# Kernel optimization log

Hardware: AMD Instinct MI355X
Metric: run time of the kernel (lower is better)

The kernel has to match this reference:

```python
import jax, jax.numpy as jnp
import numpy as np

EPS = 1e-3  # BatchNorm eps from module init
N, C_IN, K = 200000, 256, 27
C_MID = C_IN // 4  # bottleneck expansion = 4


def batch_norm(h, gamma, beta):
    # BatchNorm1d in training mode: biased batch stats over the node dim
    mean = jnp.mean(h, axis=0)
    var = jnp.var(h, axis=0)
    return (h - mean) * jax.lax.rsqrt(var + EPS) * gamma + beta


def setup_inputs() -> dict:
    key = jax.random.key(0)
    ks = jax.random.split(key, 8)
    x = jax.random.normal(ks[0], (N, C_IN), dtype=jnp.float32)
    neigh = jax.random.randint(ks[1], (N, K), 0, N)  # 27-neighbor octree table
    # conv weights (no bias; BN follows). Fan-in scaled init.
    W1 = jax.random.normal(ks[2], (C_IN, C_MID), dtype=jnp.float32) / np.sqrt(C_IN)
    W2 = jax.random.normal(ks[3], (K, C_MID, C_MID), dtype=jnp.float32) / np.sqrt(K * C_MID)
    W3 = jax.random.normal(ks[4], (C_MID, C_IN), dtype=jnp.float32) / np.sqrt(C_MID)
    g1 = jnp.ones((C_MID,), jnp.float32); b1 = jnp.zeros((C_MID,), jnp.float32)
    g2 = jnp.ones((C_MID,), jnp.float32); b2 = jnp.zeros((C_MID,), jnp.float32)
    g3 = jnp.ones((C_IN,), jnp.float32); b3 = jnp.zeros((C_IN,), jnp.float32)
    return {"x": x, "neigh": neigh, "depth": 6,
            "W1": W1, "g1": g1, "b1": b1,
            "W2": W2, "g2": g2, "b2": b2,
            "W3": W3, "g3": g3, "b3": b3}


def reference(x, neigh, depth, W1, g1, b1, W2, g2, b2, W3, g3, b3):
    identity = x
    # conv_bn_relu1: 1x1 octree conv -> BN -> ReLU
    h = jax.nn.relu(batch_norm(x @ W1, g1, b1))  # [N, C_MID]
    # conv_bn_relu2: 3x3 octree conv (27-neighbor gather) -> BN -> ReLU
    gathered = h[neigh]                          # [N, 27, C_MID] irregular gather
    h = jnp.einsum('nkc,kcd->nd', gathered, W2)  # [N, C_MID]
    h = jax.nn.relu(batch_norm(h, g2, b2))
    # conv3: 1x1 octree conv back to C_IN, then BN + residual + ReLU
    h = batch_norm(h @ W3, g3, b3)               # [N, C_IN]
    return jax.nn.relu(h + identity)
```

## Files before the change

### kernel.cpp

```cpp
#include <hip/hip_runtime.h>
#include <stdint.h>

#define N_NODES 200000
#define C_INN   256
#define C_MIDD  64
#define KNB     27

typedef unsigned short u16;
typedef __attribute__((ext_vector_type(8))) short short8;
typedef __attribute__((ext_vector_type(4))) float floatx4;

__device__ inline float bf2f(u16 u) {
  union { uint32_t i; float f; } v; v.i = ((uint32_t)u) << 16; return v.f;
}
__device__ inline u16 f2bf(float f) {
  union { float f; uint32_t i; } v; v.f = f;
  uint32_t lsb = (v.i >> 16) & 1u;
  uint32_t r = v.i + 0x7fffu + lsb;
  return (u16)(r >> 16);
}

__global__ void prep_kernel(const float* __restrict__ W1, const float* __restrict__ W2,
                            const float* __restrict__ W3,
                            u16* __restrict__ w1t, u16* __restrict__ w2t,
                            u16* __restrict__ w3t, float* __restrict__ stats) {
  int tid = blockIdx.x * blockDim.x + threadIdx.x;
  int nth = gridDim.x * blockDim.x;
  for (int i = tid; i < 1536; i += nth) stats[i] = 0.f;
  for (int i = tid; i < 256 * 64; i += nth) {
    int d = i >> 8, k = i & 255;
    w1t[i] = f2bf(W1[k * 64 + d]);
  }
  for (int i = tid; i < 27 * 64 * 64; i += nth) {
    int kn = i >> 12, r = i & 4095, d = r >> 6, c = r & 63;
    w2t[i] = f2bf(W2[kn * 4096 + c * 64 + d]);
  }
  for (int i = tid; i < 256 * 64; i += nth) {
    int d = i >> 6, k = i & 63;
    w3t[i] = f2bf(W3[k * 256 + d]);
  }
}

#define PAD1 136
__global__ __launch_bounds__(256) void gemm1_kernel(const float* __restrict__ x,
                                                    const u16* __restrict__ w1t,
                                                    u16* __restrict__ y1) {
  __shared__ u16 Als[64 * PAD1];
  __shared__ u16 Bls[64 * PAD1];
  int t = threadIdx.x;
  long long rowBase = (long long)blockIdx.x * 64;
  int w = t >> 6, lane = t & 63;
  int m = lane & 15, q = lane >> 4;
  floatx4 acc[4] = {};

  for (int kh = 0; kh < 2; kh++) {
    if (kh) __syncthreads();
    #pragma unroll
    for (int j = 0; j < 8; j++) {
      int lin = j * 256 + t;
      int r = lin >> 5, c4 = lin & 31;
      floatx4 v = ((const floatx4*)x)[(rowBase + r) * 64 + kh * 32 + c4];
      ushort4 u;
      u.x = f2bf(v[0]); u.y = f2bf(v[1]); u.z = f2bf(v[2]); u.w = f2bf(v[3]);
      *(ushort4*)&Als[r * PAD1 + c4 * 4] = u;
    }
    #pragma unroll
    for (int j = 0; j < 4; j++) {
      int lin = j * 256 + t;
      int n = lin >> 4, c8 = lin & 15;
      uint4 u = ((const uint4*)w1t)[n * 32 + kh * 16 + c8];
      *(uint4*)&Bls[n * PAD1 + c8 * 8] = u;
    }
    __syncthreads();
    #pragma unroll
    for (int kc = 0; kc < 4; kc++) {
      short8 af = *(const short8*)&Als[(w * 16 + m) * PAD1 + kc * 32 + q * 8];
      #pragma unroll
      for (int tt = 0; tt < 4; tt++) {
        short8 bf = *(const short8*)&Bls[(tt * 16 + m) * PAD1 + kc * 32 + q * 8];
        acc[tt] = __builtin_amdgcn_mfma_f32_16x16x32_bf16(af, bf, acc[tt], 0, 0, 0);
      }
    }
  }
  long long base = rowBase + w * 16;
  #pragma unroll
  for (int tt = 0; tt < 4; tt++)
    #pragma unroll
    for (int r = 0; r < 4; r++)
      y1[(base + q * 4 + r) * 64 + tt * 16 + m] = f2bf(acc[tt][r]);
}

#define PAD2 72
__global__ __launch_bounds__(256) void gemm2_kernel(const u16* __restrict__ h1,
                                                    const int* __restrict__ neigh,
                                                    const u16* __restrict__ w2t,
                                                    u16* __restrict__ y2) {
  __shared__ u16 Als[64 * PAD2];
  __shared__ u16 Bls[64 * PAD2];
  __shared__ int nidx[64 * 27];
  int t = threadIdx.x;
  long long rowBase = (long long)blockIdx.x * 64;
  #pragma unroll
  for (int j = 0; j < 7; j++) {
    int lin = j * 256 + t;
    if (lin < 64 * 27) nidx[lin] = neigh[rowBase * 27 + lin];
  }
  int w = t >> 6, lane = t & 63;
  int m = lane & 15, q = lane >> 4;
  floatx4 acc[4] = {};

  for (int k = 0; k < KNB; k++) {
    __syncthreads();
    #pragma unroll
    for (int j = 0; j < 2; j++) {
      int lin = j * 256 + t;
      int r = lin >> 3, c8 = lin & 7;
      long long src = (long long)nidx[r * 27 + k] * 8 + c8;
      *(uint4*)&Als[r * PAD2 + c8 * 8] = ((const uint4*)h1)[src];
      *(uint4*)&Bls[r * PAD2 + c8 * 8] = ((const uint4*)w2t)[k * 512 + lin];
    }
    __syncthreads();
    #pragma unroll
    for (int kc = 0; kc < 2; kc++) {
      short8 af = *(const short8*)&Als[(w * 16 + m) * PAD2 + kc * 32 + q * 8];
      #pragma unroll
      for (int tt = 0; tt < 4; tt++) {
        short8 bf = *(const short8*)&Bls[(tt * 16 + m) * PAD2 + kc * 32 + q * 8];
        acc[tt] = __builtin_amdgcn_mfma_f32_16x16x32_bf16(af, bf, acc[tt], 0, 0, 0);
      }
    }
  }
  long long base = rowBase + w * 16;
  #pragma unroll
  for (int tt = 0; tt < 4; tt++)
    #pragma unroll
    for (int r = 0; r < 4; r++)
      y2[(base + q * 4 + r) * 64 + tt * 16 + m] = f2bf(acc[tt][r]);
}

#define PAD3 72
__global__ __launch_bounds__(256) void gemm3_kernel(const u16* __restrict__ h2,
                                                    const u16* __restrict__ w3t,
                                                    float* __restrict__ y3) {
  __shared__ u16 Als[64 * PAD3];
  __shared__ u16 Bls[256 * PAD3];
  int t = threadIdx.x;
  long long rowBase = (long long)blockIdx.x * 64;
  #pragma unroll
  for (int j = 0; j < 2; j++) {
    int lin = j * 256 + t;
    int r = lin >> 3, c8 = lin & 7;
    *(uint4*)&Als[r * PAD3 + c8 * 8] = ((const uint4*)h2)[rowBase * 8 + lin];
  }
  #pragma unroll
  for (int j = 0; j < 8; j++) {
    int lin = j * 256 + t;
    int n = lin >> 3, c8 = lin & 7;
    *(uint4*)&Bls[n * PAD3 + c8 * 8] = ((const uint4*)w3t)[lin];
  }
  __syncthreads();
  int w = t >> 6, lane = t & 63;
  int m = lane & 15, q = lane >> 4;
  floatx4 acc[16] = {};
  short8 af0 = *(const short8*)&Als[(w * 16 + m) * PAD3 + q * 8];
  short8 af1 = *(const short8*)&Als[(w * 16 + m) * PAD3 + 32 + q * 8];
  #pragma unroll
  for (int tt = 0; tt < 16; tt++) {
    short8 b0 = *(const short8*)&Bls[(tt * 16 + m) * PAD3 + q * 8];
    short8 b1 = *(const short8*)&Bls[(tt * 16 + m) * PAD3 + 32 + q * 8];
    acc[tt] = __builtin_amdgcn_mfma_f32_16x16x32_bf16(af0, b0, acc[tt], 0, 0, 0);
    acc[tt] = __builtin_amdgcn_mfma_f32_16x16x32_bf16(af1, b1, acc[tt], 0, 0, 0);
  }
  long long base = rowBase + w * 16;
  #pragma unroll
  for (int tt = 0; tt < 16; tt++)
    #pragma unroll
    for (int r = 0; r < 4; r++)
      y3[(base + q * 4 + r) * 256 + tt * 16 + m] = acc[tt][r];
}

template <int C, bool BF>
__global__ __launch_bounds__(256) void stats_kernel(const void* __restrict__ yv,
                                                    float* __restrict__ sums) {
  const int RPB = 256 / C;
  int t = threadIdx.x;
  int c = t % C, rg = t / C;
  float s = 0.f, sq = 0.f;
  for (long long row = (long long)blockIdx.x * RPB + rg; row < N_NODES;
       row += (long long)gridDim.x * RPB) {
    float v = BF ? bf2f(((const u16*)yv)[row * C + c])
                 : ((const float*)yv)[row * C + c];
    s += v; sq += v * v;
  }
  __shared__ float ls[256], lq[256];
  ls[t] = s; lq[t] = sq;
  __syncthreads();
  if (t < C) {
    float S = 0.f, Q = 0.f;
    for (int g = 0; g < RPB; g++) { S += ls[g * C + t]; Q += lq[g * C + t]; }
    atomicAdd(&sums[t], S);
    atomicAdd(&sums[C + t], Q);
  }
}

__global__ void finalize_kernel(const float* __restrict__ sums, const float* __restrict__ g,
                                const float* __restrict__ b, float* __restrict__ ac, int C) {
  int t = threadIdx.x;
  if (t < C) {
    float inv = 1.f / (float)N_NODES;
    float mean = sums[t] * inv;
    float var = sums[C + t] * inv - mean * mean;
    float a = g[t] * rsqrtf(var + 1e-3f);
    ac[t] = a;
    ac[C + t] = b[t] - mean * a;
  }
}

__global__ __launch_bounds__(256) void apply_bn_relu_kernel(u16* __restrict__ y,
                                                            const float* __restrict__ ac) {
  __shared__ float a[64], cc[64];
  int t = threadIdx.x;
  if (t < 64) { a[t] = ac[t]; cc[t] = ac[64 + t]; }
  __syncthreads();
  const long long total = (long long)N_NODES * 64 / 8;
  for (long long i = (long long)blockIdx.x * 256 + t; i < total;
       i += (long long)gridDim.x * 256) {
    uint4 u = ((uint4*)y)[i];
    int c0 = (int)((i & 7) * 8);
    u16* us = (u16*)&u;
    #pragma unroll
    for (int j = 0; j < 8; j++) {
      float v = bf2f(us[j]);
      v = fmaf(a[c0 + j], v, cc[c0 + j]);
      us[j] = f2bf(fmaxf(v, 0.f));
    }
    ((uint4*)y)[i] = u;
  }
}

__global__ __launch_bounds__(256) void epilogue_kernel(float* __restrict__ y3,
                                                       const float* __restrict__ x,
                                                       const float* __restrict__ ac) {
  __shared__ float a[256], cc[256];
  int t = threadIdx.x;
  a[t] = ac[t]; cc[t] = ac[256 + t];
  __syncthreads();
  const long long total = (long long)N_NODES * 256 / 4;
  for (long long i = (long long)blockIdx.x * 256 + t; i < total;
       i += (long long)gridDim.x * 256) {
    floatx4 v = ((floatx4*)y3)[i];
    floatx4 xi = ((const floatx4*)x)[i];
    int c0 = (int)((i & 63) * 4);
    #pragma unroll
    for (int j = 0; j < 4; j++) {
      float r = fmaf(a[c0 + j], v[j], cc[c0 + j]) + xi[j];
      v[j] = fmaxf(r, 0.f);
    }
    ((floatx4*)y3)[i] = v;
  }
}

extern "C" void kernel_launch(void* const* d_in, const int* in_sizes, int n_in,
                              void* d_out, int out_size, void* d_ws, size_t ws_size,
                              hipStream_t stream) {
  (void)in_sizes; (void)n_in; (void)out_size; (void)ws_size;
  const float* x  = (const float*)d_in[0];
  const int* neigh = (const int*)d_in[1];
  const float* W1 = (const float*)d_in[3];
  const float* g1 = (const float*)d_in[4];
  const float* b1 = (const float*)d_in[5];
  const float* W2 = (const float*)d_in[6];
  const float* g2 = (const float*)d_in[7];
  const float* b2 = (const float*)d_in[8];
  const float* W3 = (const float*)d_in[9];
  const float* g3 = (const float*)d_in[10];
  const float* b3 = (const float*)d_in[11];

  char* ws = (char*)d_ws;
  u16* h1  = (u16*)(ws);
  u16* h2  = (u16*)(ws + 25600000LL);
  u16* w1t = (u16*)(ws + 51200000LL);
  u16* w2t = (u16*)(ws + 51232768LL);
  u16* w3t = (u16*)(ws + 51453952LL);
  float* stats = (float*)(ws + 51486720LL);
  float* s1 = stats,        *ac1 = stats + 128;
  float* s2 = stats + 256,  *ac2 = stats + 384;
  float* s3 = stats + 512,  *ac3 = stats + 1024;
  float* y3 = (float*)d_out;

  const int MB = N_NODES / 64;

  prep_kernel<<<256, 256, 0, stream>>>(W1, W2, W3, w1t, w2t, w3t, stats);

  gemm1_kernel<<<MB, 256, 0, stream>>>(x, w1t, h1);
  stats_kernel<64, true><<<1024, 256, 0, stream>>>(h1, s1);
  finalize_kernel<<<1, 256, 0, stream>>>(s1, g1, b1, ac1, 64);
  apply_bn_relu_kernel<<<2048, 256, 0, stream>>>(h1, ac1);

  gemm2_kernel<<<MB, 256, 0, stream>>>(h1, neigh, w2t, h2);
  stats_kernel<64, true><<<1024, 256, 0, stream>>>(h2, s2);
  finalize_kernel<<<1, 256, 0, stream>>>(s2, g2, b2, ac2, 64);
  apply_bn_relu_kernel<<<2048, 256, 0, stream>>>(h2, ac2);

  gemm3_kernel<<<MB, 256, 0, stream>>>(h2, w3t, y3);
  stats_kernel<256, false><<<2048, 256, 0, stream>>>(y3, s3);
  finalize_kernel<<<1, 256, 0, stream>>>(s3, g3, b3, ac3, 256);
  epilogue_kernel<<<4096, 256, 0, stream>>>(y3, x, ac3);
}
```

Baseline: 764.2 us.

## Fuse BN stats into GEMMs and derive BN3 stats from Gram matrix

```diff
diff --git a/kernel.cpp b/kernel.cpp
--- a/kernel.cpp
+++ b/kernel.cpp
@@ -5,6 +5,8 @@
 #define C_INN   256
 #define C_MIDD  64
 #define KNB     27
+#define MB_TILES 3125
+#define GRAM_BLOCKS 512
 
 typedef unsigned short u16;
 typedef __attribute__((ext_vector_type(8))) short short8;
@@ -26,7 +28,7 @@
                             u16* __restrict__ w3t, float* __restrict__ stats) {
   int tid = blockIdx.x * blockDim.x + threadIdx.x;
   int nth = gridDim.x * blockDim.x;
-  for (int i = tid; i < 1536; i += nth) stats[i] = 0.f;
+  for (int i = tid; i < 512; i += nth) stats[i] = 0.f;
   for (int i = tid; i < 256 * 64; i += nth) {
     int d = i >> 8, k = i & 255;
     w1t[i] = f2bf(W1[k * 64 + d]);
@@ -44,7 +46,8 @@
 #define PAD1 136
 __global__ __launch_bounds__(256) void gemm1_kernel(const float* __restrict__ x,
                                                     const u16* __restrict__ w1t,
-                                                    u16* __restrict__ y1) {
+                                                    u16* __restrict__ y1,
+                                                    float* __restrict__ s) {
   __shared__ u16 Als[64 * PAD1];
   __shared__ u16 Bls[64 * PAD1];
   int t = threadIdx.x;
@@ -88,13 +91,43 @@
     #pragma unroll
     for (int r = 0; r < 4; r++)
       y1[(base + q * 4 + r) * 64 + tt * 16 + m] = f2bf(acc[tt][r]);
+
+  float sv[4], qv[4];
+  #pragma unroll
+  for (int tt = 0; tt < 4; tt++) {
+    float sl = 0.f, ql = 0.f;
+    #pragma unroll
+    for (int r = 0; r < 4; r++) { float v = acc[tt][r]; sl += v; ql += v * v; }
+    sl += __shfl_xor(sl, 16); sl += __shfl_xor(sl, 32);
+    ql += __shfl_xor(ql, 16); ql += __shfl_xor(ql, 32);
+    sv[tt] = sl; qv[tt] = ql;
+  }
+  __syncthreads();
+  float* sred = (float*)Als;
+  float* qred = sred + 256;
+  if (q == 0) {
+    #pragma unroll
+    for (int tt = 0; tt < 4; tt++) {
+      sred[w * 64 + tt * 16 + m] = sv[tt];
+      qred[w * 64 + tt * 16 + m] = qv[tt];
+    }
+  }
+  __syncthreads();
+  if (t < 64) {
+    float S = 0.f, Q = 0.f;
+    #pragma unroll
+    for (int g = 0; g < 4; g++) { S += sred[g * 64 + t]; Q += qred[g * 64 + t]; }
+    atomicAdd(&s[t], S);
+    atomicAdd(&s[64 + t], Q);
+  }
 }
 
 #define PAD2 72
 __global__ __launch_bounds__(256) void gemm2_kernel(const u16* __restrict__ h1,
                                                     const int* __restrict__ neigh,
                                                     const u16* __restrict__ w2t,
-                                                    u16* __restrict__ y2) {
+                                                    u16* __restrict__ y2,
+                                                    float* __restrict__ s) {
   __shared__ u16 Als[64 * PAD2];
   __shared__ u16 Bls[64 * PAD2];
   __shared__ int nidx[64 * 27];
@@ -136,70 +169,34 @@
     #pragma unroll
     for (int r = 0; r < 4; r++)
       y2[(base + q * 4 + r) * 64 + tt * 16 + m] = f2bf(acc[tt][r]);
-}
-
-#define PAD3 72
-__global__ __launch_bounds__(256) void gemm3_kernel(const u16* __restrict__ h2,
-                                                    const u16* __restrict__ w3t,
-                                                    float* __restrict__ y3) {
-  __shared__ u16 Als[64 * PAD3];
-  __shared__ u16 Bls[256 * PAD3];
-  int t = threadIdx.x;
-  long long rowBase = (long long)blockIdx.x * 64;
-  #pragma unroll
-  for (int j = 0; j < 2; j++) {
-    int lin = j * 256 + t;
-    int r = lin >> 3, c8 = lin & 7;
-    *(uint4*)&Als[r * PAD3 + c8 * 8] = ((const uint4*)h2)[rowBase * 8 + lin];
-  }
-  #pragma unroll
-  for (int j = 0; j < 8; j++) {
-    int lin = j * 256 + t;
-    int n = lin >> 3, c8 = lin & 7;
-    *(uint4*)&Bls[n * PAD3 + c8 * 8] = ((const uint4*)w3t)[lin];
-  }
-  __syncthreads();
-  int w = t >> 6, lane = t & 63;
-  int m = lane & 15, q = lane >> 4;
-  floatx4 acc[16] = {};
-  short8 af0 = *(const short8*)&Als[(w * 16 + m) * PAD3 + q * 8];
-  short8 af1 = *(const short8*)&Als[(w * 16 + m) * PAD3 + 32 + q * 8];
-  #pragma unroll
-  for (int tt = 0; tt < 16; tt++) {
-    short8 b0 = *(const short8*)&Bls[(tt * 16 + m) * PAD3 + q * 8];
-    short8 b1 = *(const short8*)&Bls[(tt * 16 + m) * PAD3 + 32 + q * 8];
-    acc[tt] = __builtin_amdgcn_mfma_f32_16x16x32_bf16(af0, b0, acc[tt], 0, 0, 0);
-    acc[tt] = __builtin_amdgcn_mfma_f32_16x16x32_bf16(af1, b1, acc[tt], 0, 0, 0);
-  }
-  long long base = rowBase + w * 16;
-  #pragma unroll
-  for (int tt = 0; tt < 16; tt++)
-    #pragma unroll
-    for (int r = 0; r < 4; r++)
-      y3[(base + q * 4 + r) * 256 + tt * 16 + m] = acc[tt][r];
-}
-
-template <int C, bool BF>
-__global__ __launch_bounds__(256) void stats_kernel(const void* __restrict__ yv,
-                                                    float* __restrict__ sums) {
-  const int RPB = 256 / C;
-  int t = threadIdx.x;
-  int c = t % C, rg = t / C;
-  float s = 0.f, sq = 0.f;
-  for (long long row = (long long)blockIdx.x * RPB + rg; row < N_NODES;
-       row += (long long)gridDim.x * RPB) {
-    float v = BF ? bf2f(((const u16*)yv)[row * C + c])
-                 : ((const float*)yv)[row * C + c];
-    s += v; sq += v * v;
-  }
-  __shared__ float ls[256], lq[256];
-  ls[t] = s; lq[t] = sq;
-  __syncthreads();
-  if (t < C) {
+
+  float sv[4], qv[4];
+  #pragma unroll
+  for (int tt = 0; tt < 4; tt++) {
+    float sl = 0.f, ql = 0.f;
+    #pragma unroll
+    for (int r = 0; r < 4; r++) { float v = acc[tt][r]; sl += v; ql += v * v; }
+    sl += __shfl_xor(sl, 16); sl += __shfl_xor(sl, 32);
+    ql += __shfl_xor(ql, 16); ql += __shfl_xor(ql, 32);
+    sv[tt] = sl; qv[tt] = ql;
+  }
+  __syncthreads();
+  float* sred = (float*)Als;
+  float* qred = sred + 256;
+  if (q == 0) {
+    #pragma unroll
+    for (int tt = 0; tt < 4; tt++) {
+      sred[w * 64 + tt * 16 + m] = sv[tt];
+      qred[w * 64 + tt * 16 + m] = qv[tt];
+    }
+  }
+  __syncthreads();
+  if (t < 64) {
     float S = 0.f, Q = 0.f;
-    for (int g = 0; g < RPB; g++) { S += ls[g * C + t]; Q += lq[g * C + t]; }
-    atomicAdd(&sums[t], S);
-    atomicAdd(&sums[C + t], Q);
+    #pragma unroll
+    for (int g = 0; g < 4; g++) { S += sred[g * 64 + t]; Q += qred[g * 64 + t]; }
+    atomicAdd(&s[t], S);
+    atomicAdd(&s[64 + t], Q);
   }
 }
 
@@ -238,25 +235,154 @@
   }
 }
 
-__global__ __launch_bounds__(256) void epilogue_kernel(float* __restrict__ y3,
-                                                       const float* __restrict__ x,
-                                                       const float* __restrict__ ac) {
-  __shared__ float a[256], cc[256];
-  int t = threadIdx.x;
-  a[t] = ac[t]; cc[t] = ac[256 + t];
-  __syncthreads();
-  const long long total = (long long)N_NODES * 256 / 4;
-  for (long long i = (long long)blockIdx.x * 256 + t; i < total;
-       i += (long long)gridDim.x * 256) {
-    floatx4 v = ((floatx4*)y3)[i];
-    floatx4 xi = ((const floatx4*)x)[i];
-    int c0 = (int)((i & 63) * 4);
-    #pragma unroll
-    for (int j = 0; j < 4; j++) {
-      float r = fmaf(a[c0 + j], v[j], cc[c0 + j]) + xi[j];
-      v[j] = fmaxf(r, 0.f);
-    }
-    ((floatx4*)y3)[i] = v;
+#define PADG 72
+__global__ __launch_bounds__(256) void gram_kernel(const u16* __restrict__ h2,
+                                                   float* __restrict__ Gpart,
+                                                   float* __restrict__ cspart) {
+  __shared__ u16 T[64 * PADG];
+  int t = threadIdx.x;
+  int w = t >> 6, lane = t & 63;
+  int m = lane & 15, q = lane >> 4;
+  const int c8 = t & 7;
+  floatx4 acc[4] = {};
+  float csl[8] = {};
+  for (int tile = blockIdx.x; tile < MB_TILES; tile += gridDim.x) {
+    __syncthreads();
+    #pragma unroll
+    for (int j = 0; j < 2; j++) {
+      int lin = j * 256 + t;
+      int r = lin >> 3;
+      uint4 u = ((const uint4*)h2)[(long long)tile * 512 + lin];
+      u16* us = (u16*)&u;
+      #pragma unroll
+      for (int e = 0; e < 8; e++) {
+        csl[e] += bf2f(us[e]);
+        T[(c8 * 8 + e) * PADG + r] = us[e];
+      }
+    }
+    __syncthreads();
+    #pragma unroll
+    for (int kc = 0; kc < 2; kc++) {
+      short8 af = *(const short8*)&T[(w * 16 + m) * PADG + kc * 32 + q * 8];
+      #pragma unroll
+      for (int tt = 0; tt < 4; tt++) {
+        short8 bf = *(const short8*)&T[(tt * 16 + m) * PADG + kc * 32 + q * 8];
+        acc[tt] = __builtin_amdgcn_mfma_f32_16x16x32_bf16(af, bf, acc[tt], 0, 0, 0);
+      }
+    }
+  }
+  long long b = blockIdx.x;
+  #pragma unroll
+  for (int tt = 0; tt < 4; tt++)
+    #pragma unroll
+    for (int r = 0; r < 4; r++)
+      Gpart[b * 4096 + (w * 16 + q * 4 + r) * 64 + tt * 16 + m] = acc[tt][r];
+  __syncthreads();
+  float* cred = (float*)T;
+  #pragma unroll
+  for (int e = 0; e < 8; e++) cred[t * 8 + e] = csl[e];
+  __syncthreads();
+  if (t < 64) {
+    float S = 0.f;
+    for (int g = 0; g < 32; g++) S += cred[((g << 3) | (t >> 3)) * 8 + (t & 7)];
+    cspart[b * 64 + t] = S;
+  }
+}
+
+__global__ void greduce_kernel(const float* __restrict__ Gpart,
+                               const float* __restrict__ cspart,
+                               float* __restrict__ G, float* __restrict__ cs) {
+  int idx = blockIdx.x * 64 + threadIdx.x;
+  if (idx < 4096) {
+    float S = 0.f;
+    for (int b = 0; b < GRAM_BLOCKS; b++) S += Gpart[b * 4096 + idx];
+    G[idx] = S;
+  } else if (idx < 4160) {
+    int c = idx - 4096;
+    float S = 0.f;
+    for (int b = 0; b < GRAM_BLOCKS; b++) S += cspart[b * 64 + c];
+    cs[c] = S;
+  }
+}
+
+__global__ void finalize3_kernel(const float* __restrict__ G, const float* __restrict__ cs,
+                                 const u16* __restrict__ w3t, const float* __restrict__ g3,
+                                 const float* __restrict__ b3, float* __restrict__ ac3) {
+  __shared__ float Gs[4096];
+  __shared__ float css[64];
+  int t = threadIdx.x;
+  for (int i = t; i < 4096; i += 256) Gs[i] = G[i];
+  if (t < 64) css[t] = cs[t];
+  __syncthreads();
+  float wv[64];
+  #pragma unroll
+  for (int k = 0; k < 64; k++) wv[k] = bf2f(w3t[t * 64 + k]);
+  const float invN = 1.f / (float)N_NODES;
+  float mean = 0.f;
+  #pragma unroll
+  for (int k = 0; k < 64; k++) mean += css[k] * wv[k];
+  mean *= invN;
+  float qf = 0.f;
+  #pragma unroll
+  for (int k = 0; k < 64; k++) {
+    float tmp = 0.f;
+    #pragma unroll
+    for (int k2 = 0; k2 < 64; k2++) tmp += Gs[k * 64 + k2] * wv[k2];
+    qf += wv[k] * tmp;
+  }
+  float var = qf * invN - mean * mean;
+  float a = g3[t] * rsqrtf(var + 1e-3f);
+  ac3[t] = a;
+  ac3[256 + t] = b3[t] - mean * a;
+}
+
+#define PAD3 72
+__global__ __launch_bounds__(256) void gemm3e_kernel(const u16* __restrict__ h2,
+                                                     const u16* __restrict__ w3t,
+                                                     const float* __restrict__ ac,
+                                                     const float* __restrict__ x,
+                                                     float* __restrict__ out) {
+  __shared__ u16 Als[64 * PAD3];
+  __shared__ u16 Bls[256 * PAD3];
+  __shared__ float aS[256], cS[256];
+  int t = threadIdx.x;
+  aS[t] = ac[t]; cS[t] = ac[256 + t];
+  long long rowBase = (long long)blockIdx.x * 64;
+  #pragma unroll
+  for (int j = 0; j < 2; j++) {
+    int lin = j * 256 + t;
+    int r = lin >> 3, c8 = lin & 7;
+    *(uint4*)&Als[r * PAD3 + c8 * 8] = ((const uint4*)h2)[rowBase * 8 + lin];
+  }
+  #pragma unroll
+  for (int j = 0; j < 8; j++) {
+    int lin = j * 256 + t;
+    int n = lin >> 3, c8 = lin & 7;
+    *(uint4*)&Bls[n * PAD3 + c8 * 8] = ((const uint4*)w3t)[lin];
+  }
+  __syncthreads();
+  int w = t >> 6, lane = t & 63;
+  int m = lane & 15, q = lane >> 4;
+  floatx4 acc[16] = {};
+  short8 af0 = *(const short8*)&Als[(w * 16 + m) * PAD3 + q * 8];
+  short8 af1 = *(const short8*)&Als[(w * 16 + m) * PAD3 + 32 + q * 8];
+  #pragma unroll
+  for (int tt = 0; tt < 16; tt++) {
+    short8 b0 = *(const short8*)&Bls[(tt * 16 + m) * PAD3 + q * 8];
+    short8 b1 = *(const short8*)&Bls[(tt * 16 + m) * PAD3 + 32 + q * 8];
+    acc[tt] = __builtin_amdgcn_mfma_f32_16x16x32_bf16(af0, b0, acc[tt], 0, 0, 0);
+    acc[tt] = __builtin_amdgcn_mfma_f32_16x16x32_bf16(af1, b1, acc[tt], 0, 0, 0);
+  }
+  long long base = rowBase + w * 16;
+  #pragma unroll
+  for (int r = 0; r < 4; r++) {
+    long long row = base + q * 4 + r;
+    #pragma unroll
+    for (int tt = 0; tt < 16; tt++) {
+      int col = tt * 16 + m;
+      float v = fmaf(aS[col], acc[tt][r], cS[col]) + x[row * 256 + col];
+      out[row * 256 + col] = fmaxf(v, 0.f);
+    }
   }
 }
 
@@ -283,27 +409,27 @@
   u16* w2t = (u16*)(ws + 51232768LL);
   u16* w3t = (u16*)(ws + 51453952LL);
   float* stats = (float*)(ws + 51486720LL);
-  float* s1 = stats,        *ac1 = stats + 128;
-  float* s2 = stats + 256,  *ac2 = stats + 384;
-  float* s3 = stats + 512,  *ac3 = stats + 1024;
-  float* y3 = (float*)d_out;
-
-  const int MB = N_NODES / 64;
+  float* s1  = stats,       *ac1 = stats + 128;
+  float* s2  = stats + 256, *ac2 = stats + 384;
+  float* G   = stats + 512;
+  float* cs3 = stats + 4608;
+  float* ac3 = stats + 4672;
+  float* Gpart  = (float*)(ws + 51507456LL);
+  float* cspart = (float*)(ws + 59896064LL);
+  float* out = (float*)d_out;
 
   prep_kernel<<<256, 256, 0, stream>>>(W1, W2, W3, w1t, w2t, w3t, stats);
 
-  gemm1_kernel<<<MB, 256, 0, stream>>>(x, w1t, h1);
-  stats_kernel<64, true><<<1024, 256, 0, stream>>>(h1, s1);
+  gemm1_kernel<<<MB_TILES, 256, 0, stream>>>(x, w1t, h1, s1);
   finalize_kernel<<<1, 256, 0, stream>>>(s1, g1, b1, ac1, 64);
   apply_bn_relu_kernel<<<2048, 256, 0, stream>>>(h1, ac1);
 
-  gemm2_kernel<<<MB, 256, 0, stream>>>(h1, neigh, w2t, h2);
-  stats_kernel<64, true><<<1024, 256, 0, stream>>>(h2, s2);
+  gemm2_kernel<<<MB_TILES, 256, 0, stream>>>(h1, neigh, w2t, h2, s2);
   finalize_kernel<<<1, 256, 0, stream>>>(s2, g2, b2, ac2, 64);
   apply_bn_relu_kernel<<<2048, 256, 0, stream>>>(h2, ac2);
 
-  gemm3_kernel<<<MB, 256, 0, stream>>>(h2, w3t, y3);
-  stats_kernel<256, false><<<2048, 256, 0, stream>>>(y3, s3);
-  finalize_kernel<<<1, 256, 0, stream>>>(s3, g3, b3, ac3, 256);
-  epilogue_kernel<<<4096, 256, 0, stream>>>(y3, x, ac3);
-}
+  gram_kernel<<<GRAM_BLOCKS, 256, 0, stream>>>(h2, Gpart, cspart);
+  greduce_kernel<<<65, 64, 0, stream>>>(Gpart, cspart, G, cs3);
+  finalize3_kernel<<<1, 256, 0, stream>>>(G, cs3, w3t, g3, b3, ac3);
+  gemm3e_kernel<<<MB_TILES, 256, 0, stream>>>(h2, w3t, ac3, x, out);
+}
```

After: 836.4 us. +9.5%, slower.
